# Kernel optimization log

Hardware: AMD Instinct MI355X
Metric: run time of the kernel (lower is better)

Reference implementation:

```python
import jax, jax.numpy as jnp
import numpy as np

B, N, D, S, H = 32, 4096, 256, 16, 512
ITERS = 3
EPS = 1e-8
LN_EPS = 1e-5  # torch LayerNorm default


def _ln(x, w, b):
    m = jnp.mean(x, axis=-1, keepdims=True)
    v = jnp.mean(jnp.square(x - m), axis=-1, keepdims=True)
    return (x - m) / jnp.sqrt(v + LN_EPS) * w + b


def setup_inputs() -> dict:
    key = jax.random.key(0)
    ks = jax.random.split(key, 20)
    s = 1.0 / np.sqrt(D)
    return {
        "inputs": jax.random.normal(ks[0], (B, N, D), jnp.float32),
        "token_weight": jax.random.uniform(ks[1], (B, N), jnp.float32),
        "noise": jax.random.normal(ks[2], (B, S, D), jnp.float32),
        "ln_in_w": jnp.ones((D,), jnp.float32), "ln_in_b": jnp.zeros((D,), jnp.float32),
        "ln_s_w": jnp.ones((D,), jnp.float32), "ln_s_b": jnp.zeros((D,), jnp.float32),
        "ln_m_w": jnp.ones((D,), jnp.float32), "ln_m_b": jnp.zeros((D,), jnp.float32),
        "Wk": jax.random.normal(ks[3], (D, D), jnp.float32) * s,
        "Wv": jax.random.normal(ks[4], (D, D), jnp.float32) * s,
        "Wq": jax.random.normal(ks[5], (D, D), jnp.float32) * s,
        "gru_wih": jax.random.normal(ks[6], (3 * D, D), jnp.float32) * s,
        "gru_whh": jax.random.normal(ks[7], (3 * D, D), jnp.float32) * s,
        "gru_bih": jax.random.normal(ks[8], (3 * D,), jnp.float32) * s,
        "gru_bhh": jax.random.normal(ks[9], (3 * D,), jnp.float32) * s,
        "mlp_w1": jax.random.normal(ks[10], (H, D), jnp.float32) * s,
        "mlp_b1": jnp.zeros((H,), jnp.float32),
        "mlp_w2": jax.random.normal(ks[11], (D, H), jnp.float32) * (1.0 / np.sqrt(H)),
        "mlp_b2": jnp.zeros((D,), jnp.float32),
        "slots_mu": jax.random.normal(ks[12], (1, 1, D), jnp.float32) * 0.02,
        "slots_logsigma": jax.random.normal(ks[13], (1, 1, D), jnp.float32) * 0.02,
    }


def _gru(x, h, wih, whh, bih, bhh):
    # torch GRUCell: gates ordered r, z, n
    gi = x @ wih.T + bih  # [BS, 3D]
    gh = h @ whh.T + bhh
    ir, iz, inn = jnp.split(gi, 3, axis=-1)
    hr, hz, hn = jnp.split(gh, 3, axis=-1)
    r = jax.nn.sigmoid(ir + hr)
    z = jax.nn.sigmoid(iz + hz)
    n = jnp.tanh(inn + r * hn)
    return (1.0 - z) * n + z * h


def reference(inputs, token_weight, noise, ln_in_w, ln_in_b, ln_s_w, ln_s_b,
              ln_m_w, ln_m_b, Wk, Wv, Wq, gru_wih, gru_whh, gru_bih, gru_bhh,
              mlp_w1, mlp_b1, mlp_w2, mlp_b2, slots_mu, slots_logsigma):
    tw = jnp.clip(token_weight, 0.0, None)  # [B,N]
    x = _ln(inputs, ln_in_w, ln_in_b)
    k = x @ Wk.T  # [B,N,D]
    v = x @ Wv.T
    sigma = jnp.clip(jnp.exp(slots_logsigma), 1e-6, None)
    slots = slots_mu + sigma * noise  # [B,S,D]
    scale = D ** (-0.5)
    attn = None
    for _ in range(ITERS):
        slots_prev = slots
        q = _ln(slots, ln_s_w, ln_s_b) @ Wq.T  # [B,S,D]
        logits = jnp.einsum('bnd,bmd->bnm', k, q) * scale  # [B,N,S]
        attn = jax.nn.softmax(logits, axis=-1)  # softmax over slots
        attn = attn * tw[:, :, None]
        attn = attn / (jnp.sum(attn, axis=1, keepdims=True) + EPS)  # normalize over tokens
        updates = jnp.einsum('bnm,bnd->bmd', attn, v)  # [B,S,D]
        slots = _gru(updates.reshape(B * S, D), slots_prev.reshape(B * S, D),
                     gru_wih, gru_whh, gru_bih, gru_bhh).reshape(B, S, D)
        h = jax.nn.gelu(_ln(slots, ln_m_w, ln_m_b) @ mlp_w1.T + mlp_b1, approximate=False)
        slots = slots + h @ mlp_w2.T + mlp_b2
    return slots, attn
```

## Files before the change

kernel.cpp:

```cpp
#include <hip/hip_runtime.h>
#include <hip/hip_bf16.h>
#include <math.h>


#define EPS_ 1e-8f
#define LNEPS_ 1e-5f

typedef __attribute__((ext_vector_type(8))) short bf16x8;
typedef __attribute__((ext_vector_type(4))) float f32x4;
typedef __attribute__((ext_vector_type(4))) short s16x4;

static __device__ __forceinline__ short f2bf(float f) {
  __hip_bfloat16 h = __float2bfloat16(f);
  union { __hip_bfloat16 h; short s; } u; u.h = h; return u.s;
}
static __device__ __forceinline__ float4 ld4(const float* p){ return *(const float4*)p; }

template<int OBF>
__global__ __launch_bounds__(256) void k_ln_row(const float* __restrict__ in,
    const float* __restrict__ w, const float* __restrict__ b, void* __restrict__ out) {
  int row  = blockIdx.x*4 + (threadIdx.x>>6);
  int lane = threadIdx.x & 63;
  float4 v = ld4(in + (size_t)row*256 + lane*4);
  float s  = v.x+v.y+v.z+v.w;
  float sq = v.x*v.x+v.y*v.y+v.z*v.z+v.w*v.w;
  #pragma unroll
  for (int d=1; d<64; d<<=1) { s += __shfl_xor(s,d); sq += __shfl_xor(sq,d); }
  float mean = s*(1.f/256.f);
  float rstd = rsqrtf(sq*(1.f/256.f) - mean*mean + LNEPS_);
  float4 wv = ld4(w + lane*4), bv = ld4(b + lane*4);
  float o0 = (v.x-mean)*rstd*wv.x + bv.x;
  float o1 = (v.y-mean)*rstd*wv.y + bv.y;
  float o2 = (v.z-mean)*rstd*wv.z + bv.z;
  float o3 = (v.w-mean)*rstd*wv.w + bv.w;
  if (OBF) {
    short4 o; o.x=f2bf(o0); o.y=f2bf(o1); o.z=f2bf(o2); o.w=f2bf(o3);
    *(short4*)((short*)out + (size_t)row*256 + lane*4) = o;
  } else {
    float4 o = make_float4(o0,o1,o2,o3);
    *(float4*)((float*)out + (size_t)row*256 + lane*4) = o;
  }
}

__global__ __launch_bounds__(256) void k_mt(const float* __restrict__ Wq,
    const float* __restrict__ Wk, short* __restrict__ MT) {
  int e = blockIdx.x, f = threadIdx.x;
  float acc = 0.f;
  #pragma unroll 4
  for (int d=0; d<256; d++) acc += Wq[d*256+f]*Wk[d*256+e];
  MT[e*256+f] = f2bf(acc);
}

__global__ __launch_bounds__(256) void k_cast5(
    const float* __restrict__ a0, const float* __restrict__ a1,
    const float* __restrict__ a2, const float* __restrict__ a3,
    const float* __restrict__ a4,
    short* __restrict__ o0, short* __restrict__ o1, short* __restrict__ o2,
    short* __restrict__ o3, short* __restrict__ o4) {
  int c = blockIdx.x*256 + threadIdx.x;
  const float* src; short* dst;
  if (c < 16384) { src=a0; dst=o0; }
  else if ((c-=16384) < 49152) { src=a1; dst=o1; }
  else if ((c-=49152) < 49152) { src=a2; dst=o2; }
  else if ((c-=49152) < 32768) { src=a3; dst=o3; }
  else { c-=32768; src=a4; dst=o4; }
  float4 v = ld4(src + (size_t)c*4);
  short4 o; o.x=f2bf(v.x); o.y=f2bf(v.y); o.z=f2bf(v.z); o.w=f2bf(v.w);
  *(short4*)(dst + (size_t)c*4) = o;
}

__global__ __launch_bounds__(256) void k_slots_init(const float* __restrict__ mu,
    const float* __restrict__ ls, const float* __restrict__ noise,
    float* __restrict__ slots, short* __restrict__ slotsb) {
  int i = blockIdx.x*256 + threadIdx.x;
  int d = (i*4) & 255;
  float4 nz = ld4(noise + (size_t)i*4);
  float4 m  = ld4(mu + d);
  float4 l  = ld4(ls + d);
  float4 o;
  o.x = m.x + fmaxf(__expf(l.x),1e-6f)*nz.x;
  o.y = m.y + fmaxf(__expf(l.y),1e-6f)*nz.y;
  o.z = m.z + fmaxf(__expf(l.z),1e-6f)*nz.z;
  o.w = m.w + fmaxf(__expf(l.w),1e-6f)*nz.w;
  *(float4*)(slots + (size_t)i*4) = o;
  short4 ob; ob.x=f2bf(o.x); ob.y=f2bf(o.y); ob.z=f2bf(o.z); ob.w=f2bf(o.w);
  *(short4*)(slotsb + (size_t)i*4) = ob;
}

__global__ __launch_bounds__(256) void k3_fused(
    const short* __restrict__ x, const short* __restrict__ qk,
    const float* __restrict__ twg, float* __restrict__ ux_part,
    float* __restrict__ colsum_part, float* __restrict__ attn_un, int write_attn) {
  __shared__ short Xs[64*264];
  __shared__ short QKs[16*264];
  __shared__ short Pt[16*72];
  __shared__ float tws[64];
  __shared__ float cs[16];
  const int t = threadIdx.x;
  const int b = blockIdx.x >> 4;
  const int n0 = (blockIdx.x & 15) * 256;
  const int lane = t & 63;
  const int w = t >> 6;
  const int l15 = lane & 15;
  const int lg  = lane >> 4;
  #pragma unroll
  for (int i=0;i<2;i++){
    int cid = t + i*256;
    int row = cid>>5, ck = cid&31;
    *(uint4*)&QKs[row*264 + ck*8] = *(const uint4*)&qk[((size_t)(b*16+row))*256 + ck*8];
  }
  if (t<16) cs[t]=0.f;
  f32x4 uacc[4] = {};
  for (int g=0; g<4; ++g) {
    __syncthreads();
    const short* xg = x + ((size_t)b*4096 + n0 + g*64)*256;
    #pragma unroll
    for (int r8=0;r8<8;r8++){
      int row = r8*8 + (t>>5), ck = t&31;
      *(uint4*)&Xs[row*264 + ck*8] = *(const uint4*)&xg[(size_t)row*256 + ck*8];
    }
    if (t<64) tws[t] = fmaxf(twg[(size_t)b*4096 + n0 + g*64 + t], 0.f);
    __syncthreads();
    f32x4 acc = {0.f,0.f,0.f,0.f};
    #pragma unroll
    for (int kk=0;kk<8;kk++){
      bf16x8 af  = *(const bf16x8*)&Xs[(w*16+l15)*264 + kk*32 + lg*8];
      bf16x8 bfr = *(const bf16x8*)&QKs[l15*264 + kk*32 + lg*8];
      acc = __builtin_amdgcn_mfma_f32_16x16x32_bf16(af, bfr, acc, 0,0,0);
    }
    float a4[4];
    #pragma unroll
    for (int q=0;q<4;q++){
      float v = acc[q]*0.0625f;
      float m = v;
      #pragma unroll
      for (int d=1; d<16; d<<=1) m = fmaxf(m, __shfl_xor(m, d, 16));
      float e = __expf(v-m);
      float se = e;
      #pragma unroll
      for (int d=1; d<16; d<<=1) se += __shfl_xor(se, d, 16);
      int row = w*16 + lg*4 + q;
      float a = (e/se)*tws[row];
      a4[q] = a;
      if (write_attn)
        attn_un[((size_t)b*4096 + n0 + g*64 + row)*16 + l15] = a;
    }
    float psum = a4[0]+a4[1]+a4[2]+a4[3];
    psum += __shfl_xor(psum, 16);
    psum += __shfl_xor(psum, 32);
    if (lane<16) atomicAdd(&cs[l15], psum);
    s16x4 pk; pk[0]=f2bf(a4[0]); pk[1]=f2bf(a4[1]); pk[2]=f2bf(a4[2]); pk[3]=f2bf(a4[3]);
    *(s16x4*)&Pt[l15*72 + w*16 + lg*4] = pk;
    __syncthreads();
    #pragma unroll
    for (int kk=0;kk<2;kk++){
      bf16x8 a2 = *(const bf16x8*)&Pt[l15*72 + kk*32 + lg*8];
      #pragma unroll
      for (int tt=0;tt<4;tt++){
        int col = w*64 + tt*16 + l15;
        int rbv = kk*32 + lg*8;
        bf16x8 b2;
        #pragma unroll
        for (int j=0;j<8;j++) b2[j] = Xs[(rbv+j)*264 + col];
        uacc[tt] = __builtin_amdgcn_mfma_f32_16x16x32_bf16(a2, b2, uacc[tt], 0,0,0);
      }
    }
  }
  __syncthreads();
  if (t<16) colsum_part[blockIdx.x*16 + t] = cs[t];
  #pragma unroll
  for (int tt=0;tt<4;tt++){
    #pragma unroll
    for (int q=0;q<4;q++)
      ux_part[(size_t)blockIdx.x*4096 + (lg*4+q)*256 + w*64 + tt*16 + l15] = uacc[tt][q];
  }
}

__global__ __launch_bounds__(256) void k_reduce(const float* __restrict__ uxp,
    const float* __restrict__ csp, short* __restrict__ uxr, float* __restrict__ csr) {
  int r = blockIdx.x;
  int b = r>>4, s = r&15;
  int t = threadIdx.x;
  float cs = 0.f;
  #pragma unroll
  for (int k=0;k<16;k++) cs += csp[((b<<4)+k)*16 + s];
  float u = 0.f;
  #pragma unroll
  for (int k=0;k<16;k++) u += uxp[(size_t)((b<<4)+k)*4096 + s*256 + t];
  uxr[(size_t)r*256+t] = f2bf(u/(cs+EPS_));
  if (t==0) csr[r] = cs;
}

template<int EPI, int ZSEL>
__global__ __launch_bounds__(256) void k_mgemm(
    const short* __restrict__ A, const short* __restrict__ W,
    const float* __restrict__ bias, const float* __restrict__ res,
    float* __restrict__ outf, short* __restrict__ outb,
    const short* __restrict__ A2, const short* __restrict__ W2,
    const float* __restrict__ bias2, int K, int ldc) {
  __shared__ short As[64*56];
  __shared__ short Ws[64*56];
  if (ZSEL && blockIdx.z) { A=A2; W=W2; bias=bias2; outf += 768; }
  const int t = threadIdx.x;
  const int bm = blockIdx.y, bn = blockIdx.x;
  const int w = t>>6, lane = t&63, l15 = lane&15, lg = lane>>4;
  const int srow = t>>2, scol = (t&3)*8;
  f32x4 acc[4] = {};
  for (int k0=0; k0<K; k0+=32) {
    __syncthreads();
    *(uint4*)&As[srow*56 + scol] = *(const uint4*)&A[(size_t)(bm*64+srow)*K + k0 + scol];
    *(uint4*)&Ws[srow*56 + scol] = *(const uint4*)&W[(size_t)(bn*64+srow)*K + k0 + scol];
    __syncthreads();
    bf16x8 af = *(const bf16x8*)&As[(w*16+l15)*56 + lg*8];
    #pragma unroll
    for (int ct=0; ct<4; ct++) {
      bf16x8 bfr = *(const bf16x8*)&Ws[(ct*16+l15)*56 + lg*8];
      acc[ct] = __builtin_amdgcn_mfma_f32_16x16x32_bf16(af, bfr, acc[ct], 0,0,0);
    }
  }
  #pragma unroll
  for (int ct=0; ct<4; ct++) {
    int col = bn*64 + ct*16 + l15;
    float bv = bias ? bias[col] : 0.f;
    #pragma unroll
    for (int q=0; q<4; q++) {
      int row = bm*64 + w*16 + lg*4 + q;
      float v = acc[ct][q] + bv;
      if (EPI==1) v = 0.5f*v*(1.f+erff(v*0.70710678118654752f));
      if (EPI==3) v += res[(size_t)row*ldc + col];
      if (EPI==0 || EPI==1) {
        outb[(size_t)row*ldc + col] = f2bf(v);
      } else {
        outf[(size_t)row*ldc + col] = v;
        if (EPI==3) outb[(size_t)row*ldc + col] = f2bf(v);
      }
    }
  }
}

__global__ __launch_bounds__(256) void k_gates(const float* __restrict__ gig,
    const float* __restrict__ lw, const float* __restrict__ lb,
    float* __restrict__ slots, short* __restrict__ lnmb) {
  int row  = blockIdx.x*4 + (threadIdx.x>>6);
  int lane = threadIdx.x & 63;
  const float* gi = gig + (size_t)row*1536 + lane*4;
  float4 ir = ld4(gi), iz = ld4(gi+256), inn = ld4(gi+512);
  float4 hr = ld4(gi+768), hz = ld4(gi+1024), hn = ld4(gi+1280);
  float* sp = slots + (size_t)row*256 + lane*4;
  float4 h = ld4(sp);
  float hp[4];
  {
    float r0 = 1.f/(1.f+__expf(-(ir.x+hr.x))); float z0 = 1.f/(1.f+__expf(-(iz.x+hz.x)));
    hp[0] = (1.f-z0)*tanhf(inn.x + r0*hn.x) + z0*h.x;
    float r1 = 1.f/(1.f+__expf(-(ir.y+hr.y))); float z1 = 1.f/(1.f+__expf(-(iz.y+hz.y)));
    hp[1] = (1.f-z1)*tanhf(inn.y + r1*hn.y) + z1*h.y;
    float r2 = 1.f/(1.f+__expf(-(ir.z+hr.z))); float z2 = 1.f/(1.f+__expf(-(iz.z+hz.z)));
    hp[2] = (1.f-z2)*tanhf(inn.z + r2*hn.z) + z2*h.z;
    float r3 = 1.f/(1.f+__expf(-(ir.w+hr.w))); float z3 = 1.f/(1.f+__expf(-(iz.w+hz.w)));
    hp[3] = (1.f-z3)*tanhf(inn.w + r3*hn.w) + z3*h.w;
  }
  float s = hp[0]+hp[1]+hp[2]+hp[3];
  float sq = hp[0]*hp[0]+hp[1]*hp[1]+hp[2]*hp[2]+hp[3]*hp[3];
  #pragma unroll
  for (int d=1; d<64; d<<=1) { s += __shfl_xor(s,d); sq += __shfl_xor(sq,d); }
  float mean = s*(1.f/256.f);
  float rstd = rsqrtf(sq*(1.f/256.f) - mean*mean + LNEPS_);
  float4 wv = ld4(lw+lane*4), bv = ld4(lb+lane*4);
  *(float4*)sp = make_float4(hp[0],hp[1],hp[2],hp[3]);
  short4 o;
  o.x = f2bf((hp[0]-mean)*rstd*wv.x+bv.x);
  o.y = f2bf((hp[1]-mean)*rstd*wv.y+bv.y);
  o.z = f2bf((hp[2]-mean)*rstd*wv.z+bv.z);
  o.w = f2bf((hp[3]-mean)*rstd*wv.w+bv.w);
  *(short4*)(lnmb + (size_t)row*256 + lane*4) = o;
}

__global__ __launch_bounds__(256) void k_attn_norm(const float* __restrict__ au,
    const float* __restrict__ cs, float* __restrict__ out) {
  size_t i = ((size_t)blockIdx.x*256 + threadIdx.x)*4;
  float4 v = ld4(au + i);
  int s = (int)(i & 15);
  size_t b = i >> 16;
  const float* c = cs + b*16 + s;
  float4 o;
  o.x = v.x/(c[0]+EPS_); o.y = v.y/(c[1]+EPS_);
  o.z = v.z/(c[2]+EPS_); o.w = v.w/(c[3]+EPS_);
  *(float4*)(out + i) = o;
}

extern "C" void kernel_launch(void* const* d_in, const int* in_sizes, int n_in,
                              void* d_out, int out_size, void* d_ws, size_t ws_size,
                              hipStream_t stream) {
  const float* inputs   = (const float*)d_in[0];
  const float* token_w  = (const float*)d_in[1];
  const float* noise    = (const float*)d_in[2];
  const float* ln_in_w  = (const float*)d_in[3];
  const float* ln_in_b  = (const float*)d_in[4];
  const float* ln_s_w   = (const float*)d_in[5];
  const float* ln_s_b   = (const float*)d_in[6];
  const float* ln_m_w   = (const float*)d_in[7];
  const float* ln_m_b   = (const float*)d_in[8];
  const float* Wk       = (const float*)d_in[9];
  const float* Wv       = (const float*)d_in[10];
  const float* Wq       = (const float*)d_in[11];
  const float* gru_wih  = (const float*)d_in[12];
  const float* gru_whh  = (const float*)d_in[13];
  const float* gru_bih  = (const float*)d_in[14];
  const float* gru_bhh  = (const float*)d_in[15];
  const float* mlp_w1   = (const float*)d_in[16];
  const float* mlp_b1   = (const float*)d_in[17];
  const float* mlp_w2   = (const float*)d_in[18];
  const float* mlp_b2   = (const float*)d_in[19];
  const float* slots_mu = (const float*)d_in[20];
  const float* slots_ls = (const float*)d_in[21];

  float* out_slots = (float*)d_out;
  float* out_attn  = out_slots + 131072;

  char* wsb = (char*)d_ws;
  size_t off = 0;
  short* xbf     = (short*)(wsb + off); off += 67108864;
  float* attn_un = (float*)(wsb + off); off += 8388608;
  float* ux_part = (float*)(wsb + off); off += 8388608;
  float* cs_part = (float*)(wsb + off); off += 32768;
  float* cs_red  = (float*)(wsb + off); off += 2048;
  short* qk      = (short*)(wsb + off); off += 262144;
  short* uxr     = (short*)(wsb + off); off += 262144;
  short* MTb     = (short*)(wsb + off); off += 131072;
  short* lnS     = (short*)(wsb + off); off += 262144;
  short* updb    = (short*)(wsb + off); off += 262144;
  float* gig     = (float*)(wsb + off); off += 3145728;
  float* slots   = (float*)(wsb + off); off += 524288;
  short* slotsb  = (short*)(wsb + off); off += 262144;
  short* lnmb    = (short*)(wsb + off); off += 262144;
  short* hb      = (short*)(wsb + off); off += 524288;
  short* Wvb     = (short*)(wsb + off); off += 131072;
  short* wihb    = (short*)(wsb + off); off += 393216;
  short* whhb    = (short*)(wsb + off); off += 393216;
  short* w1b     = (short*)(wsb + off); off += 262144;
  short* w2b     = (short*)(wsb + off); off += 262144;

  k_mt<<<256,256,0,stream>>>(Wq, Wk, MTb);
  k_cast5<<<704,256,0,stream>>>(Wv, gru_wih, gru_whh, mlp_w1, mlp_w2,
                                Wvb, wihb, whhb, w1b, w2b);
  k_slots_init<<<128,256,0,stream>>>(slots_mu, slots_ls, noise, slots, slotsb);
  k_ln_row<1><<<32768,256,0,stream>>>(inputs, ln_in_w, ln_in_b, (void*)xbf);

  k_ln_row<1><<<128,256,0,stream>>>(slots, ln_s_w, ln_s_b, (void*)lnS);
  k_mgemm<0,0><<<dim3(4,8),256,0,stream>>>(lnS, MTb, nullptr, nullptr, nullptr, qk,
                                           nullptr, nullptr, nullptr, 256, 256);
  for (int it=0; it<3; ++it) {
    k3_fused<<<512,256,0,stream>>>(xbf, qk, token_w, ux_part, cs_part, attn_un, it==2 ? 1:0);
    k_reduce<<<512,256,0,stream>>>(ux_part, cs_part, uxr, cs_red);
    k_mgemm<0,0><<<dim3(4,8),256,0,stream>>>(uxr, Wvb, nullptr, nullptr, nullptr, updb,
                                             nullptr, nullptr, nullptr, 256, 256);
    k_mgemm<2,1><<<dim3(12,8,2),256,0,stream>>>(updb, wihb, gru_bih, nullptr, gig, nullptr,
                                                slotsb, whhb, gru_bhh, 256, 1536);
    k_gates<<<128,256,0,stream>>>(gig, ln_m_w, ln_m_b, slots, lnmb);
    k_mgemm<1,0><<<dim3(8,8),256,0,stream>>>(lnmb, w1b, mlp_b1, nullptr, nullptr, hb,
                                             nullptr, nullptr, nullptr, 256, 512);
    float* cdst = (it==2) ? out_slots : slots;
    k_mgemm<3,0><<<dim3(4,8),256,0,stream>>>(hb, w2b, mlp_b2, slots, cdst, slotsb,
                                             nullptr, nullptr, nullptr, 512, 256);
    if (it<2) {
      k_ln_row<1><<<128,256,0,stream>>>(slots, ln_s_w, ln_s_b, (void*)lnS);
      k_mgemm<0,0><<<dim3(4,8),256,0,stream>>>(lnS, MTb, nullptr, nullptr, nullptr, qk,
                                               nullptr, nullptr, nullptr, 256, 256);
    }
  }
  k_attn_norm<<<2048,256,0,stream>>>(attn_un, cs_red, out_attn);
}
```

Measured before the change: 257.3 us.

## Fuse input LayerNorm into attention kernel, fold Wv into GRU weights, merge slot tail

The input LayerNorm is now computed inside the first attention pass. That pass writes the bf16 normalized tokens for later iterations, so the separate full-size LN pass over the inputs goes away. Wv is pre-multiplied into gru_wih (M = wih·Wv), which removes one GEMM per iteration. The gi and gh GEMMs share a single launch. The MLP second GEMM, residual add, slot LayerNorm and q projection are fused into one 8-block kernel, and a prep kernel merges the weight setup kernels. The goal is fewer launches and less memory traffic. The cost is a low-parallelism tail kernel (8 blocks) and extra rounding from the folded weight product.

After: 241.3 us. -6.2%, faster.

```diff
diff --git a/kernel.cpp b/kernel.cpp
--- a/kernel.cpp
+++ b/kernel.cpp
@@ -16,110 +16,114 @@
 }
 static __device__ __forceinline__ float4 ld4(const float* p){ return *(const float4*)p; }
 
-template<int OBF>
-__global__ __launch_bounds__(256) void k_ln_row(const float* __restrict__ in,
-    const float* __restrict__ w, const float* __restrict__ b, void* __restrict__ out) {
-  int row  = blockIdx.x*4 + (threadIdx.x>>6);
-  int lane = threadIdx.x & 63;
-  float4 v = ld4(in + (size_t)row*256 + lane*4);
-  float s  = v.x+v.y+v.z+v.w;
-  float sq = v.x*v.x+v.y*v.y+v.z*v.z+v.w*v.w;
-  #pragma unroll
-  for (int d=1; d<64; d<<=1) { s += __shfl_xor(s,d); sq += __shfl_xor(sq,d); }
-  float mean = s*(1.f/256.f);
-  float rstd = rsqrtf(sq*(1.f/256.f) - mean*mean + LNEPS_);
-  float4 wv = ld4(w + lane*4), bv = ld4(b + lane*4);
-  float o0 = (v.x-mean)*rstd*wv.x + bv.x;
-  float o1 = (v.y-mean)*rstd*wv.y + bv.y;
-  float o2 = (v.z-mean)*rstd*wv.z + bv.z;
-  float o3 = (v.w-mean)*rstd*wv.w + bv.w;
-  if (OBF) {
-    short4 o; o.x=f2bf(o0); o.y=f2bf(o1); o.z=f2bf(o2); o.w=f2bf(o3);
-    *(short4*)((short*)out + (size_t)row*256 + lane*4) = o;
+__global__ __launch_bounds__(256) void k_prep(
+    const float* __restrict__ Wq, const float* __restrict__ Wk,
+    const float* __restrict__ wih, const float* __restrict__ Wv,
+    const float* __restrict__ whh, const float* __restrict__ w1, const float* __restrict__ w2,
+    short* __restrict__ MTb, short* __restrict__ Mb, short* __restrict__ whhb,
+    short* __restrict__ w1b, short* __restrict__ w2b) {
+  int blk = blockIdx.x, t = threadIdx.x;
+  if (blk < 64) {
+    int e0 = blk*4;
+    float a0=0,a1=0,a2=0,a3=0;
+    for (int d=0; d<256; d++) {
+      float qv = Wq[d*256 + t];
+      a0 += qv*Wk[d*256+e0];   a1 += qv*Wk[d*256+e0+1];
+      a2 += qv*Wk[d*256+e0+2]; a3 += qv*Wk[d*256+e0+3];
+    }
+    MTb[(e0  )*256+t]=f2bf(a0); MTb[(e0+1)*256+t]=f2bf(a1);
+    MTb[(e0+2)*256+t]=f2bf(a2); MTb[(e0+3)*256+t]=f2bf(a3);
+  } else if (blk < 256) {
+    int n0 = (blk-64)*4;
+    float a0=0,a1=0,a2=0,a3=0;
+    for (int d=0; d<256; d++) {
+      float vv = Wv[d*256 + t];
+      a0 += wih[(n0  )*256+d]*vv; a1 += wih[(n0+1)*256+d]*vv;
+      a2 += wih[(n0+2)*256+d]*vv; a3 += wih[(n0+3)*256+d]*vv;
+    }
+    Mb[(size_t)(n0  )*256+t]=f2bf(a0); Mb[(size_t)(n0+1)*256+t]=f2bf(a1);
+    Mb[(size_t)(n0+2)*256+t]=f2bf(a2); Mb[(size_t)(n0+3)*256+t]=f2bf(a3);
   } else {
-    float4 o = make_float4(o0,o1,o2,o3);
-    *(float4*)((float*)out + (size_t)row*256 + lane*4) = o;
-  }
-}
-
-__global__ __launch_bounds__(256) void k_mt(const float* __restrict__ Wq,
-    const float* __restrict__ Wk, short* __restrict__ MT) {
-  int e = blockIdx.x, f = threadIdx.x;
-  float acc = 0.f;
-  #pragma unroll 4
-  for (int d=0; d<256; d++) acc += Wq[d*256+f]*Wk[d*256+e];
-  MT[e*256+f] = f2bf(acc);
-}
-
-__global__ __launch_bounds__(256) void k_cast5(
-    const float* __restrict__ a0, const float* __restrict__ a1,
-    const float* __restrict__ a2, const float* __restrict__ a3,
-    const float* __restrict__ a4,
-    short* __restrict__ o0, short* __restrict__ o1, short* __restrict__ o2,
-    short* __restrict__ o3, short* __restrict__ o4) {
-  int c = blockIdx.x*256 + threadIdx.x;
-  const float* src; short* dst;
-  if (c < 16384) { src=a0; dst=o0; }
-  else if ((c-=16384) < 49152) { src=a1; dst=o1; }
-  else if ((c-=49152) < 49152) { src=a2; dst=o2; }
-  else if ((c-=49152) < 32768) { src=a3; dst=o3; }
-  else { c-=32768; src=a4; dst=o4; }
-  float4 v = ld4(src + (size_t)c*4);
-  short4 o; o.x=f2bf(v.x); o.y=f2bf(v.y); o.z=f2bf(v.z); o.w=f2bf(v.w);
-  *(short4*)(dst + (size_t)c*4) = o;
-}
-
-__global__ __launch_bounds__(256) void k_slots_init(const float* __restrict__ mu,
-    const float* __restrict__ ls, const float* __restrict__ noise,
-    float* __restrict__ slots, short* __restrict__ slotsb) {
-  int i = blockIdx.x*256 + threadIdx.x;
-  int d = (i*4) & 255;
-  float4 nz = ld4(noise + (size_t)i*4);
-  float4 m  = ld4(mu + d);
-  float4 l  = ld4(ls + d);
-  float4 o;
-  o.x = m.x + fmaxf(__expf(l.x),1e-6f)*nz.x;
-  o.y = m.y + fmaxf(__expf(l.y),1e-6f)*nz.y;
-  o.z = m.z + fmaxf(__expf(l.z),1e-6f)*nz.z;
-  o.w = m.w + fmaxf(__expf(l.w),1e-6f)*nz.w;
-  *(float4*)(slots + (size_t)i*4) = o;
-  short4 ob; ob.x=f2bf(o.x); ob.y=f2bf(o.y); ob.z=f2bf(o.z); ob.w=f2bf(o.w);
-  *(short4*)(slotsb + (size_t)i*4) = ob;
-}
-
-__global__ __launch_bounds__(256) void k3_fused(
-    const short* __restrict__ x, const short* __restrict__ qk,
-    const float* __restrict__ twg, float* __restrict__ ux_part,
-    float* __restrict__ colsum_part, float* __restrict__ attn_un, int write_attn) {
+    int c = (blk-256)*256 + t;
+    const float* src; short* dst;
+    if (c < 49152) { src=whh; dst=whhb; }
+    else if ((c-=49152) < 32768) { src=w1; dst=w1b; }
+    else { c-=32768; src=w2; dst=w2b; }
+    float4 v = ld4(src + (size_t)c*4);
+    short4 o; o.x=f2bf(v.x); o.y=f2bf(v.y); o.z=f2bf(v.z); o.w=f2bf(v.w);
+    *(short4*)(dst + (size_t)c*4) = o;
+  }
+}
+
+template<int LNIN, int WATTN>
+__global__ __launch_bounds__(256) void k3(
+    const float* __restrict__ inputs, const float* __restrict__ lnw, const float* __restrict__ lnb,
+    short* __restrict__ xbf, const short* __restrict__ qk, const float* __restrict__ twg,
+    float* __restrict__ ux_part, float* __restrict__ colsum_part, float* __restrict__ attn_un) {
   __shared__ short Xs[64*264];
   __shared__ short QKs[16*264];
   __shared__ short Pt[16*72];
   __shared__ float tws[64];
   __shared__ float cs[16];
+  __shared__ float lnwb[512];
   const int t = threadIdx.x;
   const int b = blockIdx.x >> 4;
   const int n0 = (blockIdx.x & 15) * 256;
-  const int lane = t & 63;
-  const int w = t >> 6;
-  const int l15 = lane & 15;
-  const int lg  = lane >> 4;
+  const int lane = t & 63, w = t >> 6, l15 = lane & 15, lg = lane >> 4;
   #pragma unroll
   for (int i=0;i<2;i++){
     int cid = t + i*256;
     int row = cid>>5, ck = cid&31;
     *(uint4*)&QKs[row*264 + ck*8] = *(const uint4*)&qk[((size_t)(b*16+row))*256 + ck*8];
   }
+  if (LNIN){
+    if (t < 64)       *(float4*)&lnwb[t*4]           = ld4(lnw + t*4);
+    else if (t < 128) *(float4*)&lnwb[256+(t-64)*4]  = ld4(lnb + (t-64)*4);
+  }
   if (t<16) cs[t]=0.f;
   f32x4 uacc[4] = {};
   for (int g=0; g<4; ++g) {
     __syncthreads();
-    const short* xg = x + ((size_t)b*4096 + n0 + g*64)*256;
-    #pragma unroll
-    for (int r8=0;r8<8;r8++){
-      int row = r8*8 + (t>>5), ck = t&31;
-      *(uint4*)&Xs[row*264 + ck*8] = *(const uint4*)&xg[(size_t)row*256 + ck*8];
-    }
-    if (t<64) tws[t] = fmaxf(twg[(size_t)b*4096 + n0 + g*64 + t], 0.f);
+    const size_t rowbase = (size_t)b*4096 + n0 + g*64;
+    if (LNIN) {
+      const float* ing = inputs + rowbase*256;
+      const int r = t>>2, c = t&3;
+      float4 vv[16];
+      #pragma unroll
+      for (int k=0;k<16;k++) vv[k] = ld4(ing + r*256 + (c+4*k)*4);
+      float s=0.f, sq=0.f;
+      #pragma unroll
+      for (int k=0;k<16;k++){
+        s  += vv[k].x+vv[k].y+vv[k].z+vv[k].w;
+        sq += vv[k].x*vv[k].x+vv[k].y*vv[k].y+vv[k].z*vv[k].z+vv[k].w*vv[k].w;
+      }
+      s += __shfl_xor(s,1);  s += __shfl_xor(s,2);
+      sq += __shfl_xor(sq,1); sq += __shfl_xor(sq,2);
+      float mean = s*(1.f/256.f);
+      float rstd = rsqrtf(sq*(1.f/256.f) - mean*mean + LNEPS_);
+      short* xw = xbf + rowbase*256;
+      #pragma unroll
+      for (int k=0;k<16;k++){
+        int d0 = (c+4*k)*4;
+        float4 wv = *(float4*)&lnwb[d0];
+        float4 bv = *(float4*)&lnwb[256+d0];
+        s16x4 pk;
+        pk[0]=f2bf((vv[k].x-mean)*rstd*wv.x+bv.x);
+        pk[1]=f2bf((vv[k].y-mean)*rstd*wv.y+bv.y);
+        pk[2]=f2bf((vv[k].z-mean)*rstd*wv.z+bv.z);
+        pk[3]=f2bf((vv[k].w-mean)*rstd*wv.w+bv.w);
+        *(s16x4*)&Xs[r*264 + d0] = pk;
+        *(s16x4*)&xw[r*256 + d0] = pk;
+      }
+    } else {
+      const short* xg = xbf + rowbase*256;
+      #pragma unroll
+      for (int r8=0;r8<8;r8++){
+        int row = r8*8 + (t>>5), ck = t&31;
+        *(uint4*)&Xs[row*264 + ck*8] = *(const uint4*)&xg[(size_t)row*256 + ck*8];
+      }
+    }
+    if (t<64) tws[t] = fmaxf(twg[rowbase + t], 0.f);
     __syncthreads();
     f32x4 acc = {0.f,0.f,0.f,0.f};
     #pragma unroll
@@ -142,8 +146,8 @@
       int row = w*16 + lg*4 + q;
       float a = (e/se)*tws[row];
       a4[q] = a;
-      if (write_attn)
-        attn_un[((size_t)b*4096 + n0 + g*64 + row)*16 + l15] = a;
+      if (WATTN)
+        attn_un[(rowbase + row)*16 + l15] = a;
     }
     float psum = a4[0]+a4[1]+a4[2]+a4[3];
     psum += __shfl_xor(psum, 16);
@@ -191,49 +195,71 @@
   if (t==0) csr[r] = cs;
 }
 
-template<int EPI, int ZSEL>
-__global__ __launch_bounds__(256) void k_mgemm(
-    const short* __restrict__ A, const short* __restrict__ W,
-    const float* __restrict__ bias, const float* __restrict__ res,
-    float* __restrict__ outf, short* __restrict__ outb,
-    const short* __restrict__ A2, const short* __restrict__ W2,
-    const float* __restrict__ bias2, int K, int ldc) {
-  __shared__ short As[64*56];
-  __shared__ short Ws[64*56];
-  if (ZSEL && blockIdx.z) { A=A2; W=W2; bias=bias2; outf += 768; }
-  const int t = threadIdx.x;
-  const int bm = blockIdx.y, bn = blockIdx.x;
-  const int w = t>>6, lane = t&63, l15 = lane&15, lg = lane>>4;
-  const int srow = t>>2, scol = (t&3)*8;
-  f32x4 acc[4] = {};
-  for (int k0=0; k0<K; k0+=32) {
-    __syncthreads();
-    *(uint4*)&As[srow*56 + scol] = *(const uint4*)&A[(size_t)(bm*64+srow)*K + k0 + scol];
-    *(uint4*)&Ws[srow*56 + scol] = *(const uint4*)&W[(size_t)(bn*64+srow)*K + k0 + scol];
-    __syncthreads();
-    bf16x8 af = *(const bf16x8*)&As[(w*16+l15)*56 + lg*8];
-    #pragma unroll
-    for (int ct=0; ct<4; ct++) {
-      bf16x8 bfr = *(const bf16x8*)&Ws[(ct*16+l15)*56 + lg*8];
-      acc[ct] = __builtin_amdgcn_mfma_f32_16x16x32_bf16(af, bfr, acc[ct], 0,0,0);
-    }
-  }
-  #pragma unroll
-  for (int ct=0; ct<4; ct++) {
-    int col = bn*64 + ct*16 + l15;
-    float bv = bias ? bias[col] : 0.f;
-    #pragma unroll
-    for (int q=0; q<4; q++) {
+__global__ __launch_bounds__(256) void k_gigh(
+    const short* __restrict__ uxr, const short* __restrict__ slotsb,
+    const short* __restrict__ Mb, const short* __restrict__ whhb,
+    const float* __restrict__ bih, const float* __restrict__ bhh,
+    float* __restrict__ gig) {
+  __shared__ short As[64*40];
+  __shared__ short Ws[64*40];
+  const int t=threadIdx.x, bn=blockIdx.x, bm=blockIdx.y;
+  const short* A; const short* W; const float* bias; int wo;
+  if (bn<12) { A=uxr;    W=Mb   + (size_t)bn*64*256;      bias=bih; wo=bn*64; }
+  else       { A=slotsb; W=whhb + (size_t)(bn-12)*64*256; bias=bhh; wo=(bn-12)*64; }
+  const int w=t>>6, lane=t&63, l15=lane&15, lg=lane>>4;
+  f32x4 acc[4]={};
+  for (int k0=0;k0<256;k0+=32){
+    __syncthreads();
+    *(uint4*)&As[(t>>2)*40+(t&3)*8] = *(const uint4*)&A[(size_t)(bm*64+(t>>2))*256 + k0 + (t&3)*8];
+    *(uint4*)&Ws[(t>>2)*40+(t&3)*8] = *(const uint4*)&W[(size_t)(t>>2)*256 + k0 + (t&3)*8];
+    __syncthreads();
+    bf16x8 af = *(const bf16x8*)&As[(w*16+l15)*40+lg*8];
+    #pragma unroll
+    for (int ct=0;ct<4;ct++){
+      bf16x8 bfr = *(const bf16x8*)&Ws[(ct*16+l15)*40+lg*8];
+      acc[ct]=__builtin_amdgcn_mfma_f32_16x16x32_bf16(af,bfr,acc[ct],0,0,0);
+    }
+  }
+  #pragma unroll
+  for (int ct=0;ct<4;ct++){
+    float bv = bias[wo + ct*16 + l15];
+    #pragma unroll
+    for (int q=0;q<4;q++){
+      int row = bm*64 + w*16 + lg*4 + q;
+      gig[(size_t)row*1536 + bn*64 + ct*16 + l15] = acc[ct][q] + bv;
+    }
+  }
+}
+
+__global__ __launch_bounds__(256) void k_mlp1(
+    const short* __restrict__ lnmb, const short* __restrict__ w1b,
+    const float* __restrict__ b1, short* __restrict__ hb) {
+  __shared__ short As[64*40];
+  __shared__ short Ws[64*40];
+  const int t=threadIdx.x, bn=blockIdx.x, bm=blockIdx.y;
+  const int w=t>>6, lane=t&63, l15=lane&15, lg=lane>>4;
+  f32x4 acc[4]={};
+  for (int k0=0;k0<256;k0+=32){
+    __syncthreads();
+    *(uint4*)&As[(t>>2)*40+(t&3)*8] = *(const uint4*)&lnmb[(size_t)(bm*64+(t>>2))*256 + k0 + (t&3)*8];
+    *(uint4*)&Ws[(t>>2)*40+(t&3)*8] = *(const uint4*)&w1b[(size_t)(bn*64+(t>>2))*256 + k0 + (t&3)*8];
+    __syncthreads();
+    bf16x8 af = *(const bf16x8*)&As[(w*16+l15)*40+lg*8];
+    #pragma unroll
+    for (int ct=0;ct<4;ct++){
+      bf16x8 bfr = *(const bf16x8*)&Ws[(ct*16+l15)*40+lg*8];
+      acc[ct]=__builtin_amdgcn_mfma_f32_16x16x32_bf16(af,bfr,acc[ct],0,0,0);
+    }
+  }
+  #pragma unroll
+  for (int ct=0;ct<4;ct++){
+    float bv = b1[bn*64 + ct*16 + l15];
+    #pragma unroll
+    for (int q=0;q<4;q++){
       int row = bm*64 + w*16 + lg*4 + q;
       float v = acc[ct][q] + bv;
-      if (EPI==1) v = 0.5f*v*(1.f+erff(v*0.70710678118654752f));
-      if (EPI==3) v += res[(size_t)row*ldc + col];
-      if (EPI==0 || EPI==1) {
-        outb[(size_t)row*ldc + col] = f2bf(v);
-      } else {
-        outf[(size_t)row*ldc + col] = v;
-        if (EPI==3) outb[(size_t)row*ldc + col] = f2bf(v);
-      }
+      v = 0.5f*v*(1.f+erff(v*0.70710678118654752f));
+      hb[(size_t)row*512 + bn*64 + ct*16 + l15] = f2bf(v);
     }
   }
 }
@@ -273,6 +299,107 @@
   o.z = f2bf((hp[2]-mean)*rstd*wv.z+bv.z);
   o.w = f2bf((hp[3]-mean)*rstd*wv.w+bv.w);
   *(short4*)(lnmb + (size_t)row*256 + lane*4) = o;
+}
+
+template<int MODE>
+__global__ __launch_bounds__(256) void k_slotend(
+    const short* __restrict__ hb, const short* __restrict__ w2b, const float* __restrict__ b2,
+    const float* __restrict__ mu, const float* __restrict__ ls, const float* __restrict__ noise,
+    const float* __restrict__ res, float* __restrict__ sout, short* __restrict__ slotsb,
+    const float* __restrict__ lnsw, const float* __restrict__ lnsb,
+    const short* __restrict__ MTb, short* __restrict__ qk) {
+  __shared__ short As[64*40];
+  __shared__ short Ws[256*40];
+  __shared__ short lnS[64*264];
+  const int t=threadIdx.x, bm=blockIdx.x;
+  const int w=t>>6, lane=t&63, l15=lane&15, lg=lane>>4;
+  float v[16][4];
+  if (MODE==1) {
+    #pragma unroll
+    for (int ct=0;ct<16;ct++){
+      int col = ct*16+l15;
+      float m = mu[col], sg = fmaxf(__expf(ls[col]),1e-6f);
+      #pragma unroll
+      for (int q=0;q<4;q++){
+        int row = bm*64 + w*16 + lg*4 + q;
+        v[ct][q] = m + sg*noise[(size_t)row*256+col];
+      }
+    }
+  } else {
+    f32x4 acc[16]={};
+    for (int k0=0;k0<512;k0+=32){
+      __syncthreads();
+      *(uint4*)&As[(t>>2)*40+(t&3)*8] = *(const uint4*)&hb[(size_t)(bm*64+(t>>2))*512 + k0 + (t&3)*8];
+      #pragma unroll
+      for (int i=0;i<4;i++){ int idx=t+i*256;
+        *(uint4*)&Ws[(idx>>2)*40+(idx&3)*8] = *(const uint4*)&w2b[(size_t)(idx>>2)*512 + k0 + (idx&3)*8]; }
+      __syncthreads();
+      bf16x8 af = *(const bf16x8*)&As[(w*16+l15)*40+lg*8];
+      #pragma unroll
+      for (int ct=0;ct<16;ct++){
+        bf16x8 bfr = *(const bf16x8*)&Ws[(ct*16+l15)*40+lg*8];
+        acc[ct]=__builtin_amdgcn_mfma_f32_16x16x32_bf16(af,bfr,acc[ct],0,0,0);
+      }
+    }
+    #pragma unroll
+    for (int ct=0;ct<16;ct++){
+      int col = ct*16+l15;
+      float bv = b2[col];
+      #pragma unroll
+      for (int q=0;q<4;q++){
+        int row = bm*64 + w*16 + lg*4 + q;
+        v[ct][q] = acc[ct][q] + bv + res[(size_t)row*256+col];
+      }
+    }
+  }
+  float s[4]={0,0,0,0}, sq[4]={0,0,0,0};
+  #pragma unroll
+  for (int ct=0;ct<16;ct++)
+    #pragma unroll
+    for (int q=0;q<4;q++){ s[q]+=v[ct][q]; sq[q]+=v[ct][q]*v[ct][q]; }
+  #pragma unroll
+  for (int q=0;q<4;q++){
+    #pragma unroll
+    for (int d=1; d<16; d<<=1){ s[q]+=__shfl_xor(s[q],d,16); sq[q]+=__shfl_xor(sq[q],d,16); }
+  }
+  #pragma unroll
+  for (int ct=0;ct<16;ct++){
+    int col = ct*16+l15;
+    float lw = (MODE!=2) ? lnsw[col] : 0.f;
+    float lb = (MODE!=2) ? lnsb[col] : 0.f;
+    #pragma unroll
+    for (int q=0;q<4;q++){
+      int row = bm*64 + w*16 + lg*4 + q;
+      sout[(size_t)row*256+col] = v[ct][q];
+      if (MODE!=2){
+        float mean = s[q]*(1.f/256.f);
+        float rstd = rsqrtf(sq[q]*(1.f/256.f)-mean*mean+LNEPS_);
+        slotsb[(size_t)row*256+col] = f2bf(v[ct][q]);
+        lnS[(w*16+lg*4+q)*264 + col] = f2bf((v[ct][q]-mean)*rstd*lw+lb);
+      }
+    }
+  }
+  if (MODE!=2){
+    f32x4 qa[16]={};
+    for (int k0=0;k0<256;k0+=32){
+      __syncthreads();
+      #pragma unroll
+      for (int i=0;i<4;i++){ int idx=t+i*256;
+        *(uint4*)&Ws[(idx>>2)*40+(idx&3)*8] = *(const uint4*)&MTb[(size_t)(idx>>2)*256 + k0 + (idx&3)*8]; }
+      __syncthreads();
+      bf16x8 af = *(const bf16x8*)&lnS[(w*16+l15)*264 + k0 + lg*8];
+      #pragma unroll
+      for (int ct=0;ct<16;ct++){
+        bf16x8 bfr = *(const bf16x8*)&Ws[(ct*16+l15)*40+lg*8];
+        qa[ct]=__builtin_amdgcn_mfma_f32_16x16x32_bf16(af,bfr,qa[ct],0,0,0);
+      }
+    }
+    #pragma unroll
+    for (int ct=0;ct<16;ct++)
+      #pragma unroll
+      for (int q=0;q<4;q++)
+        qk[(size_t)(bm*64+w*16+lg*4+q)*256 + ct*16+l15] = f2bf(qa[ct][q]);
+  }
 }
 
 __global__ __launch_bounds__(256) void k_attn_norm(const float* __restrict__ au,
@@ -327,46 +454,40 @@
   short* qk      = (short*)(wsb + off); off += 262144;
   short* uxr     = (short*)(wsb + off); off += 262144;
   short* MTb     = (short*)(wsb + off); off += 131072;
-  short* lnS     = (short*)(wsb + off); off += 262144;
-  short* updb    = (short*)(wsb + off); off += 262144;
+  short* Mb      = (short*)(wsb + off); off += 393216;
   float* gig     = (float*)(wsb + off); off += 3145728;
   float* slots   = (float*)(wsb + off); off += 524288;
   short* slotsb  = (short*)(wsb + off); off += 262144;
   short* lnmb    = (short*)(wsb + off); off += 262144;
   short* hb      = (short*)(wsb + off); off += 524288;
-  short* Wvb     = (short*)(wsb + off); off += 131072;
-  short* wihb    = (short*)(wsb + off); off += 393216;
   short* whhb    = (short*)(wsb + off); off += 393216;
   short* w1b     = (short*)(wsb + off); off += 262144;
   short* w2b     = (short*)(wsb + off); off += 262144;
 
-  k_mt<<<256,256,0,stream>>>(Wq, Wk, MTb);
-  k_cast5<<<704,256,0,stream>>>(Wv, gru_wih, gru_whh, mlp_w1, mlp_w2,
-                                Wvb, wihb, whhb, w1b, w2b);
-  k_slots_init<<<128,256,0,stream>>>(slots_mu, slots_ls, noise, slots, slotsb);
-  k_ln_row<1><<<32768,256,0,stream>>>(inputs, ln_in_w, ln_in_b, (void*)xbf);
-
-  k_ln_row<1><<<128,256,0,stream>>>(slots, ln_s_w, ln_s_b, (void*)lnS);
-  k_mgemm<0,0><<<dim3(4,8),256,0,stream>>>(lnS, MTb, nullptr, nullptr, nullptr, qk,
-                                           nullptr, nullptr, nullptr, 256, 256);
+  k_prep<<<704,256,0,stream>>>(Wq, Wk, gru_wih, Wv, gru_whh, mlp_w1, mlp_w2,
+                               MTb, Mb, whhb, w1b, w2b);
+  k_slotend<1><<<8,256,0,stream>>>(nullptr, nullptr, nullptr, slots_mu, slots_ls, noise,
+                                   nullptr, slots, slotsb, ln_s_w, ln_s_b, MTb, qk);
   for (int it=0; it<3; ++it) {
-    k3_fused<<<512,256,0,stream>>>(xbf, qk, token_w, ux_part, cs_part, attn_un, it==2 ? 1:0);
+    if (it==0)
+      k3<1,0><<<512,256,0,stream>>>(inputs, ln_in_w, ln_in_b, xbf, qk, token_w,
+                                    ux_part, cs_part, attn_un);
+    else if (it==1)
+      k3<0,0><<<512,256,0,stream>>>(inputs, ln_in_w, ln_in_b, xbf, qk, token_w,
+                                    ux_part, cs_part, attn_un);
+    else
+      k3<0,1><<<512,256,0,stream>>>(inputs, ln_in_w, ln_in_b, xbf, qk, token_w,
+                                    ux_part, cs_part, attn_un);
     k_reduce<<<512,256,0,stream>>>(ux_part, cs_part, uxr, cs_red);
-    k_mgemm<0,0><<<dim3(4,8),256,0,stream>>>(uxr, Wvb, nullptr, nullptr, nullptr, updb,
-                                             nullptr, nullptr, nullptr, 256, 256);
-    k_mgemm<2,1><<<dim3(12,8,2),256,0,stream>>>(updb, wihb, gru_bih, nullptr, gig, nullptr,
-                                                slotsb, whhb, gru_bhh, 256, 1536);
+    k_gigh<<<dim3(24,8),256,0,stream>>>(uxr, slotsb, Mb, whhb, gru_bih, gru_bhh, gig);
     k_gates<<<128,256,0,stream>>>(gig, ln_m_w, ln_m_b, slots, lnmb);
-    k_mgemm<1,0><<<dim3(8,8),256,0,stream>>>(lnmb, w1b, mlp_b1, nullptr, nullptr, hb,
-                                             nullptr, nullptr, nullptr, 256, 512);
-    float* cdst = (it==2) ? out_slots : slots;
-    k_mgemm<3,0><<<dim3(4,8),256,0,stream>>>(hb, w2b, mlp_b2, slots, cdst, slotsb,
-                                             nullptr, nullptr, nullptr, 512, 256);
-    if (it<2) {
-      k_ln_row<1><<<128,256,0,stream>>>(slots, ln_s_w, ln_s_b, (void*)lnS);
-      k_mgemm<0,0><<<dim3(4,8),256,0,stream>>>(lnS, MTb, nullptr, nullptr, nullptr, qk,
-                                               nullptr, nullptr, nullptr, 256, 256);
-    }
+    k_mlp1<<<dim3(8,8),256,0,stream>>>(lnmb, w1b, mlp_b1, hb);
+    if (it<2)
+      k_slotend<0><<<8,256,0,stream>>>(hb, w2b, mlp_b2, nullptr, nullptr, nullptr,
+                                       slots, slots, slotsb, ln_s_w, ln_s_b, MTb, qk);
+    else
+      k_slotend<2><<<8,256,0,stream>>>(hb, w2b, mlp_b2, nullptr, nullptr, nullptr,
+                                       slots, out_slots, slotsb, ln_s_w, ln_s_b, MTb, qk);
   }
   k_attn_norm<<<2048,256,0,stream>>>(attn_un, cs_red, out_attn);
 }
```
